# Optimization experiments

Hardware: AMD Instinct MI355X
Metric: run time of the kernel (lower is better)

The kernel has to match this reference:

```python
import jax, jax.numpy as jnp
import numpy as np

N = 50000
E = 800000
IN_F = 256
ATT_D = 256
H = 8
D_K = ATT_D // H  # 32
NORM_IDX = 0  # opt['attention_norm_idx']


def setup_inputs() -> dict:
    key = jax.random.key(0)
    ks = jax.random.split(key, 10)
    x = jax.random.normal(ks[0], (N, IN_F), dtype=jnp.float32)
    edge = jax.random.randint(ks[1], (2, E), 0, N, dtype=jnp.int64)
    edge_weights = jax.random.uniform(ks[2], (E,), dtype=jnp.float32)
    s = 0.02
    Wq = jax.random.normal(ks[3], (ATT_D, IN_F), dtype=jnp.float32) * s
    bq = jax.random.normal(ks[4], (ATT_D,), dtype=jnp.float32) * s
    Wk = jax.random.normal(ks[5], (ATT_D, IN_F), dtype=jnp.float32) * s
    bk = jax.random.normal(ks[6], (ATT_D,), dtype=jnp.float32) * s
    Wv = jax.random.normal(ks[7], (ATT_D, IN_F), dtype=jnp.float32) * s
    bv = jax.random.normal(ks[8], (ATT_D,), dtype=jnp.float32) * s
    return {"x": x, "edge": edge, "edge_weights": edge_weights,
            "Wq": Wq, "bq": bq, "Wk": Wk, "bk": bk, "Wv": Wv, "bv": bv}


def _segment_softmax(logits, seg, num_segments):
    # scatter-softmax grouped by seg (torch_geometric.utils.softmax semantics)
    m = jax.ops.segment_max(logits, seg, num_segments=num_segments)  # [N, H]
    ex = jnp.exp(logits - m[seg])
    s = jax.ops.segment_sum(ex, seg, num_segments=num_segments)
    return ex / (s[seg] + 1e-16)


def reference(x, edge, edge_weights, Wq, bq, Wk, bk, Wv, bv):
    # Linear projections, then [N, H, D_K] -> transpose to [N, D_K, H]
    q = (x @ Wq.T + bq).reshape(N, H, D_K).transpose(0, 2, 1)
    k = (x @ Wk.T + bk).reshape(N, H, D_K).transpose(0, 2, 1)
    v = (x @ Wv.T + bv).reshape(N, H, D_K).transpose(0, 2, 1)
    src = q[edge[0]]      # [E, D_K, H]
    dst_k = k[edge[1]]    # [E, D_K, H]
    prods = jnp.sum(src * dst_k, axis=1) / np.sqrt(D_K)  # [E, H]
    prods = prods * edge_weights[:, None]
    attention = _segment_softmax(prods, edge[NORM_IDX], N)  # [E, H]
    return attention, v
```

## Files before the change

kernel.cpp:

```cpp
#include <hip/hip_runtime.h>

#define NN 50000
#define EE 800000
#define FF 256
#define HH 8
#define DK 32

typedef short bf16x8 __attribute__((ext_vector_type(8)));
typedef float f32x4  __attribute__((ext_vector_type(4)));

__device__ __forceinline__ float b2f(short s) {
    return __uint_as_float(((unsigned)(unsigned short)s) << 16);
}
__device__ __forceinline__ short f2b(float f) {
    unsigned u = __float_as_uint(f);
    return (short)((u + 0x7fff + ((u >> 16) & 1)) >> 16);
}

__device__ __forceinline__ void gld16(void* lds, const void* g) {
    __builtin_amdgcn_global_load_lds(
        (const __attribute__((address_space(1))) unsigned int*)g,
        (__attribute__((address_space(3))) unsigned int*)lds,
        16, 0, 0);
}

__device__ __forceinline__ int xcd_swz(int bid, int nwg) {
    int q = nwg >> 3, r = nwg & 7, x = bid & 7, i = bid >> 3;
    int base = x < r ? x * (q + 1) : r * (q + 1) + (x - r) * q;
    return base + i;
}

__global__ __launch_bounds__(256) void sniff_all(
    const void* x, const void* ew, const void* wq, const void* bq,
    const void* wk, const void* bk, const void* wv, const void* bv,
    const void* edge, int* __restrict__ flags)
{
    __shared__ int tot;
    if (threadIdx.x == 0) tot = 0;
    __syncthreads();
    int b = blockIdx.x;
    if (b < 8) {
        const void* ptrs[8] = {x, ew, wq, bq, wk, bk, wv, bv};
        const int   ns[8]   = {NN * FF, EE, FF * FF, FF, FF * FF, FF, FF * FF, FF};
        const unsigned short* p = (const unsigned short*)ptrs[b];
        int half = ns[b] >> 1;
        int S = half < 4096 ? half : 4096;
        int cnt = 0;
        for (int i = threadIdx.x; i < S; i += 256) {
            unsigned v = p[2 * i];
            cnt += (((v >> 7) & 0xFF) >= 0xC0) ? 1 : 0;
        }
        atomicAdd(&tot, cnt);
        __syncthreads();
        if (threadIdx.x == 0) flags[b] = (tot * 32 > S) ? 1 : 0;
    } else {
        const unsigned* e32 = (const unsigned*)edge;
        int cnt = 0;
        for (int i = threadIdx.x; i < 4096; i += 256)
            cnt += (e32[2 * i + 1] != 0u) ? 1 : 0;
        atomicAdd(&tot, cnt);
        __syncthreads();
        if (threadIdx.x == 0) flags[8] = (tot < 100) ? 1 : 0;
    }
}

__global__ __launch_bounds__(256) void convert_wb(
    const void* wq, const void* wk, const void* wv,
    const void* bq, const void* bk, const void* bv,
    short* __restrict__ wb, float* __restrict__ bb,
    const int* __restrict__ flags)
{
    int b = blockIdx.x;
    if (b < 96) {
        int mat = b >> 5;
        const void* src = mat == 0 ? wq : mat == 1 ? wk : wv;
        int isf = flags[2 + mat * 2];
        int base = (b & 31) * 2048 + threadIdx.x * 8;
        bf16x8 v;
        if (isf) {
            const f32x4* pp = (const f32x4*)((const float*)src + base);
            f32x4 a = pp[0], c = pp[1];
            #pragma unroll
            for (int j = 0; j < 4; ++j) { v[j] = f2b(a[j]); v[4 + j] = f2b(c[j]); }
        } else {
            v = *(const bf16x8*)((const short*)src + base);
        }
        int row = base >> 8, k = base & 255;
        int s = k >> 5, quad = (k >> 3) & 3;
        int pc = (row << 2) + (quad ^ ((row >> 1) & 3));
        *(bf16x8*)(wb + mat * (FF * FF) + s * 8192 + pc * 8) = v;
    } else {
        #pragma unroll
        for (int mat = 0; mat < 3; ++mat) {
            const void* src = mat == 0 ? bq : mat == 1 ? bk : bv;
            int isf = flags[3 + mat * 2];
            int i = threadIdx.x;
            bb[mat * FF + i] = isf ? ((const float*)src)[i]
                                   : b2f(((const short*)src)[i]);
        }
    }
}

__global__ __launch_bounds__(128, 2) void qkv_gemm(
    const void* __restrict__ x, const short* __restrict__ wb,
    const float* __restrict__ bb, short* __restrict__ qo,
    short* __restrict__ ko, float* __restrict__ vo,
    const int* __restrict__ flags, int matbase, int nmats)
{
    __shared__ __align__(16) short wlds[2][8192];
    const int isf32x = flags[0];
    const int tid = threadIdx.x, wave = tid >> 6, lane = tid & 63;
    const int l16 = lane & 15, quad = lane >> 4;

    const int nwg = 782 * nmats;
    const int w = xcd_swz(blockIdx.x, nwg);
    const int xb = w / nmats;
    const int mat = matbase + (w - xb * nmats);

    const short* W = wb + mat * (FF * FF);
    const int rows0 = xb * 64 + wave * 32;

    const int rdo = l16 * 32 + ((quad ^ ((l16 >> 1) & 3)) << 3);
    const int koff = quad * 8;

    bf16x8 afrag[2][8];
    #pragma unroll
    for (int rg = 0; rg < 2; ++rg) {
        const int rowa = rows0 + rg * 16 + l16;
        const int rowc = rowa < NN ? rowa : NN - 1;
        const size_t xrow = (size_t)rowc * FF;
        if (isf32x) {
            #pragma unroll
            for (int s = 0; s < 8; ++s) {
                const f32x4* p = (const f32x4*)((const float*)x + xrow + s * 32 + koff);
                f32x4 u = p[0], v2 = p[1];
                #pragma unroll
                for (int j = 0; j < 4; ++j) {
                    afrag[rg][s][j]     = f2b(u[j]);
                    afrag[rg][s][4 + j] = f2b(v2[j]);
                }
            }
        } else {
            #pragma unroll
            for (int s = 0; s < 8; ++s)
                afrag[rg][s] = *(const bf16x8*)((const short*)x + xrow + s * 32 + koff);
        }
    }

    #define STAGE(buf, s) do {                                                  \
        const short* gs_ = W + (s) * 8192;                                      \
        _Pragma("unroll")                                                       \
        for (int i_ = 0; i_ < 8; ++i_)                                          \
            gld16(&wlds[buf][(i_ * 128 + (tid & ~63)) * 8],                     \
                  gs_ + (size_t)(i_ * 128 + tid) * 8);                          \
    } while (0)

    STAGE(0, 0);
    __syncthreads();

    f32x4 acc[2][16] = {};
    #pragma unroll
    for (int s = 0; s < 8; ++s) {
        const int cur = s & 1;
        if (s < 7) STAGE(cur ^ 1, s + 1);
        const short* ws0 = &wlds[cur][rdo];
        #pragma unroll
        for (int c = 0; c < 16; ++c) {
            bf16x8 bf = *(const bf16x8*)(ws0 + c * 512);
            acc[0][c] = __builtin_amdgcn_mfma_f32_16x16x32_bf16(afrag[0][s], bf, acc[0][c], 0, 0, 0);
            acc[1][c] = __builtin_amdgcn_mfma_f32_16x16x32_bf16(afrag[1][s], bf, acc[1][c], 0, 0, 0);
        }
        __syncthreads();
    }
    #undef STAGE

    const float* bias = bb + mat * FF;
    short* slice = (short*)wlds + wave * 8192;

    if (mat == 2) {
        float* lsf = (float*)slice;
        #pragma unroll
        for (int h = 0; h < 2; ++h) {
            #pragma unroll
            for (int rg = 0; rg < 2; ++rg)
                #pragma unroll
                for (int ci = 0; ci < 8; ++ci) {
                    int c = ci * 2 + h;
                    int col = c * 16 + l16;
                    float bv = bias[col];
                    int pcl = l16 * 8 + ci;
                    #pragma unroll
                    for (int rr = 0; rr < 4; ++rr)
                        lsf[(rg * 16 + quad * 4 + rr) * 128 + pcl] = acc[rg][c][rr] + bv;
                }
            #pragma unroll
            for (int it = 0; it < 16; ++it) {
                int idx = it * 64 + lane;
                int r = idx >> 5, cc = idx & 31;
                int row = rows0 + r;
                if (row < NN)
                    *(f32x4*)(vo + (size_t)row * FF + h * 128 + cc * 4) =
                        ((const f32x4*)lsf)[idx];
            }
        }
    } else {
        #pragma unroll
        for (int rg = 0; rg < 2; ++rg)
            #pragma unroll
            for (int c = 0; c < 16; ++c) {
                int col = c * 16 + l16;
                float bv = bias[col];
                #pragma unroll
                for (int rr = 0; rr < 4; ++rr)
                    slice[(rg * 16 + quad * 4 + rr) * 256 + col] = f2b(acc[rg][c][rr] + bv);
            }
        short* out = (mat == 0) ? qo : ko;
        #pragma unroll
        for (int it = 0; it < 16; ++it) {
            int idx = it * 64 + lane;
            int r = idx >> 5, cc = idx & 31;
            int row = rows0 + r;
            if (row < NN)
                *(bf16x8*)(out + (size_t)row * FF + cc * 8) =
                    *(const bf16x8*)(slice + r * 256 + cc * 8);
        }
    }
}

__device__ __forceinline__ float edge_exp_f(
    const int* __restrict__ edge, const void* __restrict__ ew,
    const short* __restrict__ q, const short* __restrict__ k,
    int t, int isf32, int is64, int* s_out)
{
    int e = t >> 3, h = t & 7;
    int s = is64 ? edge[2 * (size_t)e] : edge[e];
    int d = is64 ? edge[2 * ((size_t)EE + e)] : edge[EE + e];
    *s_out = s;
    const short* qp = q + (size_t)s * FF + h * DK;
    const short* kp = k + (size_t)d * FF + h * DK;
    float dot = 0.f;
    #pragma unroll
    for (int i = 0; i < 4; ++i) {
        bf16x8 qa = *(const bf16x8*)(qp + i * 8);
        bf16x8 ka = *(const bf16x8*)(kp + i * 8);
        #pragma unroll
        for (int j = 0; j < 8; ++j) dot += b2f(qa[j]) * b2f(ka[j]);
    }
    float w = isf32 ? ((const float*)ew)[e] : b2f(((const short*)ew)[e]);
    return __expf(dot * 0.17677669529663687f * w);
}

__global__ __launch_bounds__(256) void edge_pass_a(
    const int* __restrict__ edge, const void* __restrict__ ew,
    const short* __restrict__ q, const short* __restrict__ k,
    float* __restrict__ sums, float* __restrict__ expbuf,
    const int* __restrict__ flags, int use_exp)
{
    int t = blockIdx.x * 256 + threadIdx.x;
    int s;
    float exv = edge_exp_f(edge, ew, q, k, t, flags[1], flags[8], &s);
    if (use_exp) expbuf[t] = exv;
    atomicAdd(&sums[s * HH + (threadIdx.x & 7)], exv);
}

__global__ __launch_bounds__(256) void rsum_inv(float* __restrict__ sums)
{
    int i = blockIdx.x * 256 + threadIdx.x;
    if (i < NN * HH) sums[i] = 1.0f / (sums[i] + 1e-16f);
}

__global__ __launch_bounds__(256) void edge_pass_b(
    const int* __restrict__ edge, const void* __restrict__ ew,
    const short* __restrict__ q, const short* __restrict__ k,
    const float* __restrict__ sums, const float* __restrict__ expbuf,
    float* __restrict__ att, const int* __restrict__ flags, int use_exp)
{
    int t = blockIdx.x * 256 + threadIdx.x;
    float exv; int s;
    if (use_exp) {
        int e = t >> 3;
        s = flags[8] ? edge[2 * (size_t)e] : edge[e];
        exv = expbuf[t];
    } else {
        exv = edge_exp_f(edge, ew, q, k, t, flags[1], flags[8], &s);
    }
    att[t] = exv * sums[s * HH + (t & 7)];
}

extern "C" void kernel_launch(void* const* d_in, const int* in_sizes, int n_in,
                              void* d_out, int out_size, void* d_ws, size_t ws_size,
                              hipStream_t stream) {
    const void* x    = d_in[0];
    const int*  edge = (const int*)d_in[1];
    const void* ew   = d_in[2];
    const void* Wq   = d_in[3];
    const void* bq   = d_in[4];
    const void* Wk   = d_in[5];
    const void* bk   = d_in[6];
    const void* Wv   = d_in[7];
    const void* bv   = d_in[8];

    float* att_out = (float*)d_out;
    float* v_out   = att_out + (size_t)EE * HH;

    char*  ws    = (char*)d_ws;
    int*   flags = (int*)ws;
    float* sums  = (float*)(ws + 256);
    const size_t SUMS_B = (size_t)NN * HH * 4;
    const size_t Q_B    = (size_t)NN * FF * 2;
    const size_t EXP_B  = (size_t)EE * HH * 4;
    short* q_  = (short*)(ws + 256 + SUMS_B);
    short* wb  = (short*)(ws + 256 + SUMS_B + Q_B);
    float* bb  = (float*)(ws + 256 + SUMS_B + Q_B + 3 * FF * FF * 2);
    float* expb = (float*)(ws + 256 + SUMS_B + Q_B + 3 * FF * FF * 2 + 3 * FF * 4);
    const size_t BASE_B = 256 + SUMS_B + Q_B + 3 * FF * FF * 2 + 3 * FF * 4;
    const int use_exp = (ws_size >= BASE_B + EXP_B) ? 1 : 0;
    const int fused   = (ws_size >= BASE_B + EXP_B + Q_B) ? 1 : 0;

    sniff_all<<<9, 256, 0, stream>>>(x, ew, Wq, bq, Wk, bk, Wv, bv, edge, flags);
    convert_wb<<<97, 256, 0, stream>>>(Wq, Wk, Wv, bq, bk, bv, wb, bb, flags);
    hipMemsetAsync(sums, 0, SUMS_B, stream);

    const int nEH = EE * HH;

    if (fused) {
        short* k_ = (short*)(ws + BASE_B + EXP_B);
        qkv_gemm<<<782 * 3, 128, 0, stream>>>(x, wb, bb, q_, k_, v_out, flags, 0, 3);
        edge_pass_a<<<nEH / 256, 256, 0, stream>>>(edge, ew, q_, k_, sums, expb, flags, 1);
        rsum_inv<<<(NN * HH + 255) / 256, 256, 0, stream>>>(sums);
        edge_pass_b<<<nEH / 256, 256, 0, stream>>>(edge, ew, q_, k_, sums, expb, att_out, flags, 1);
    } else {
        short* k_ = (short*)v_out;
        qkv_gemm<<<782 * 2, 128, 0, stream>>>(x, wb, bb, q_, k_, nullptr, flags, 0, 2);
        edge_pass_a<<<nEH / 256, 256, 0, stream>>>(edge, ew, q_, k_, sums, expb, flags, use_exp);
        rsum_inv<<<(NN * HH + 255) / 256, 256, 0, stream>>>(sums);
        edge_pass_b<<<nEH / 256, 256, 0, stream>>>(edge, ew, q_, k_, sums, expb, att_out, flags, use_exp);
        qkv_gemm<<<782, 128, 0, stream>>>(x, wb, bb, nullptr, nullptr, v_out, flags, 2, 1);
    }
}
```

Before: 304.2 us.

## Pre-convert x to bf16 once and reuse output buffers as scratch

Adds a kernel that converts x to bf16 once. The QKV GEMMs then read the compact bf16 copy instead of converting fp32 rows in every block for each projection matrix. The exp buffer and K now live in the not-yet-written V output region, and the bf16 x copy goes in the workspace or the attention output. This removes the workspace-size-dependent fused and recompute paths, so a single schedule always runs: Q/K GEMM, the edge passes, then the V GEMM. In exchange it adds an extra full pass over x and splits the GEMM into two launches, where before there could be one.

```diff
diff --git a/kernel.cpp b/kernel.cpp
--- a/kernel.cpp
+++ b/kernel.cpp
@@ -64,6 +64,24 @@
     }
 }
 
+__global__ __launch_bounds__(256) void x_to_bf16(
+    const void* __restrict__ x, short* __restrict__ xb,
+    const int* __restrict__ flags)
+{
+    int i = blockIdx.x * 256 + threadIdx.x;
+    int base = i * 8;
+    bf16x8 v;
+    if (flags[0]) {
+        const f32x4* p = (const f32x4*)((const float*)x + base);
+        f32x4 a = p[0], c = p[1];
+        #pragma unroll
+        for (int j = 0; j < 4; ++j) { v[j] = f2b(a[j]); v[4 + j] = f2b(c[j]); }
+    } else {
+        v = *(const bf16x8*)((const short*)x + base);
+    }
+    *(bf16x8*)(xb + base) = v;
+}
+
 __global__ __launch_bounds__(256) void convert_wb(
     const void* wq, const void* wk, const void* wv,
     const void* bq, const void* bk, const void* bv,
@@ -102,10 +120,10 @@
 }
 
 __global__ __launch_bounds__(128, 2) void qkv_gemm(
-    const void* __restrict__ x, const short* __restrict__ wb,
-    const float* __restrict__ bb, short* __restrict__ qo,
-    short* __restrict__ ko, float* __restrict__ vo,
-    const int* __restrict__ flags, int matbase, int nmats)
+    const void* __restrict__ x, const short* __restrict__ xbp,
+    const short* __restrict__ wb, const float* __restrict__ bb,
+    short* __restrict__ qo, short* __restrict__ ko, float* __restrict__ vo,
+    const int* __restrict__ flags, int matbase, int nmats, int use_xb)
 {
     __shared__ __align__(16) short wlds[2][8192];
     const int isf32x = flags[0];
@@ -114,11 +132,11 @@
 
     const int nwg = 782 * nmats;
     const int w = xcd_swz(blockIdx.x, nwg);
-    const int xb = w / nmats;
-    const int mat = matbase + (w - xb * nmats);
+    const int xbk = w / nmats;
+    const int mat = matbase + (w - xbk * nmats);
 
     const short* W = wb + mat * (FF * FF);
-    const int rows0 = xb * 64 + wave * 32;
+    const int rows0 = xbk * 64 + wave * 32;
 
     const int rdo = l16 * 32 + ((quad ^ ((l16 >> 1) & 3)) << 3);
     const int koff = quad * 8;
@@ -129,7 +147,12 @@
         const int rowa = rows0 + rg * 16 + l16;
         const int rowc = rowa < NN ? rowa : NN - 1;
         const size_t xrow = (size_t)rowc * FF;
-        if (isf32x) {
+        if (use_xb) {
+            const short* xp = xbp + xrow + koff;
+            #pragma unroll
+            for (int s = 0; s < 8; ++s)
+                afrag[rg][s] = *(const bf16x8*)(xp + s * 32);
+        } else if (isf32x) {
             #pragma unroll
             for (int s = 0; s < 8; ++s) {
                 const f32x4* p = (const f32x4*)((const float*)x + xrow + s * 32 + koff);
@@ -254,12 +277,12 @@
     const int* __restrict__ edge, const void* __restrict__ ew,
     const short* __restrict__ q, const short* __restrict__ k,
     float* __restrict__ sums, float* __restrict__ expbuf,
-    const int* __restrict__ flags, int use_exp)
+    const int* __restrict__ flags)
 {
     int t = blockIdx.x * 256 + threadIdx.x;
     int s;
     float exv = edge_exp_f(edge, ew, q, k, t, flags[1], flags[8], &s);
-    if (use_exp) expbuf[t] = exv;
+    expbuf[t] = exv;
     atomicAdd(&sums[s * HH + (threadIdx.x & 7)], exv);
 }
 
@@ -270,21 +293,14 @@
 }
 
 __global__ __launch_bounds__(256) void edge_pass_b(
-    const int* __restrict__ edge, const void* __restrict__ ew,
-    const short* __restrict__ q, const short* __restrict__ k,
-    const float* __restrict__ sums, const float* __restrict__ expbuf,
-    float* __restrict__ att, const int* __restrict__ flags, int use_exp)
+    const int* __restrict__ edge, const float* __restrict__ sums,
+    const float* __restrict__ expbuf, float* __restrict__ att,
+    const int* __restrict__ flags)
 {
     int t = blockIdx.x * 256 + threadIdx.x;
-    float exv; int s;
-    if (use_exp) {
-        int e = t >> 3;
-        s = flags[8] ? edge[2 * (size_t)e] : edge[e];
-        exv = expbuf[t];
-    } else {
-        exv = edge_exp_f(edge, ew, q, k, t, flags[1], flags[8], &s);
-    }
-    att[t] = exv * sums[s * HH + (t & 7)];
+    int e = t >> 3;
+    int s = flags[8] ? edge[2 * (size_t)e] : edge[e];
+    att[t] = expbuf[t] * sums[s * HH + (t & 7)];
 }
 
 extern "C" void kernel_launch(void* const* d_in, const int* in_sizes, int n_in,
@@ -308,33 +324,30 @@
     float* sums  = (float*)(ws + 256);
     const size_t SUMS_B = (size_t)NN * HH * 4;
     const size_t Q_B    = (size_t)NN * FF * 2;
-    const size_t EXP_B  = (size_t)EE * HH * 4;
+    const size_t XB_B   = (size_t)NN * FF * 2;
     short* q_  = (short*)(ws + 256 + SUMS_B);
     short* wb  = (short*)(ws + 256 + SUMS_B + Q_B);
     float* bb  = (float*)(ws + 256 + SUMS_B + Q_B + 3 * FF * FF * 2);
-    float* expb = (float*)(ws + 256 + SUMS_B + Q_B + 3 * FF * FF * 2 + 3 * FF * 4);
     const size_t BASE_B = 256 + SUMS_B + Q_B + 3 * FF * FF * 2 + 3 * FF * 4;
-    const int use_exp = (ws_size >= BASE_B + EXP_B) ? 1 : 0;
-    const int fused   = (ws_size >= BASE_B + EXP_B + Q_B) ? 1 : 0;
+    const int xb_in_ws = (ws_size >= BASE_B + XB_B) ? 1 : 0;
+
+    short* xb = xb_in_ws ? (short*)(ws + BASE_B) : (short*)att_out;
+
+    short* k_   = (short*)v_out;
+    float* expb = v_out + (size_t)EE * HH;
 
     sniff_all<<<9, 256, 0, stream>>>(x, ew, Wq, bq, Wk, bk, Wv, bv, edge, flags);
     convert_wb<<<97, 256, 0, stream>>>(Wq, Wk, Wv, bq, bk, bv, wb, bb, flags);
+    x_to_bf16<<<NN * FF / 8 / 256, 256, 0, stream>>>(x, xb, flags);
     hipMemsetAsync(sums, 0, SUMS_B, stream);
 
     const int nEH = EE * HH;
 
-    if (fused) {
-        short* k_ = (short*)(ws + BASE_B + EXP_B);
-        qkv_gemm<<<782 * 3, 128, 0, stream>>>(x, wb, bb, q_, k_, v_out, flags, 0, 3);
-        edge_pass_a<<<nEH / 256, 256, 0, stream>>>(edge, ew, q_, k_, sums, expb, flags, 1);
-        rsum_inv<<<(NN * HH + 255) / 256, 256, 0, stream>>>(sums);
-        edge_pass_b<<<nEH / 256, 256, 0, stream>>>(edge, ew, q_, k_, sums, expb, att_out, flags, 1);
-    } else {
-        short* k_ = (short*)v_out;
-        qkv_gemm<<<782 * 2, 128, 0, stream>>>(x, wb, bb, q_, k_, nullptr, flags, 0, 2);
-        edge_pass_a<<<nEH / 256, 256, 0, stream>>>(edge, ew, q_, k_, sums, expb, flags, use_exp);
-        rsum_inv<<<(NN * HH + 255) / 256, 256, 0, stream>>>(sums);
-        edge_pass_b<<<nEH / 256, 256, 0, stream>>>(edge, ew, q_, k_, sums, expb, att_out, flags, use_exp);
-        qkv_gemm<<<782, 128, 0, stream>>>(x, wb, bb, nullptr, nullptr, v_out, flags, 2, 1);
-    }
-}
+    qkv_gemm<<<782 * 2, 128, 0, stream>>>(x, xb, wb, bb, q_, k_, nullptr,
+                                          flags, 0, 2, 1);
+    edge_pass_a<<<nEH / 256, 256, 0, stream>>>(edge, ew, q_, k_, sums, expb, flags);
+    rsum_inv<<<(NN * HH + 255) / 256, 256, 0, stream>>>(sums);
+    edge_pass_b<<<nEH / 256, 256, 0, stream>>>(edge, sums, expb, att_out, flags);
+    qkv_gemm<<<782, 128, 0, stream>>>(x, xb, wb, bb, nullptr, nullptr, v_out,
+                                      flags, 2, 1, xb_in_ws);
+}
```

New measurement: 313.0 us. 2.9% more time.
